# Kernel optimization log

Measured on AMD Instinct MI355X. Metric: run time of the kernel, lower is better.

## Reference

```python
import jax, jax.numpy as jnp
import numpy as np

B, SIG, L, LAT, ENC_H, DEC_H, RHS_H, T = 256, 64, 1024, 256, 256, 512, 512, 200


def setup_inputs() -> dict:
    key = jax.random.key(0)
    ks = jax.random.split(key, 32)
    p = lambda k, s: jax.random.normal(k, s, dtype=jnp.float32) * 0.05
    inp = {
        'y': jax.random.normal(ks[0], (B, SIG, L), dtype=jnp.float32),
        't': jnp.arange(T, dtype=jnp.float32) * 0.01,
        # encoder: conv3 (OIH) + bias, res conv1 + bias, 3 layers
        'ew0': p(ks[1], (ENC_H, SIG, 3)), 'eb0': p(ks[2], (ENC_H,)),
        'rw0': p(ks[3], (ENC_H, SIG, 1)), 'rb0': p(ks[4], (ENC_H,)),
        'ew1': p(ks[5], (ENC_H, ENC_H, 3)), 'eb1': p(ks[6], (ENC_H,)),
        'rw1': p(ks[7], (ENC_H, ENC_H, 1)), 'rb1': p(ks[8], (ENC_H,)),
        'ew2': p(ks[9], (LAT, ENC_H, 3)), 'eb2': p(ks[10], (LAT,)),
        'rw2': p(ks[11], (LAT, ENC_H, 1)), 'rb2': p(ks[12], (LAT,)),
        # rhs MLP: LAT -> RHS_H -> RHS_H -> LAT
        'fw0': p(ks[13], (RHS_H, LAT)), 'fb0': p(ks[14], (RHS_H,)),
        'fw1': p(ks[15], (RHS_H, RHS_H)), 'fb1': p(ks[16], (RHS_H,)),
        'fw2': p(ks[17], (LAT, RHS_H)), 'fb2': p(ks[18], (LAT,)),
        # decoder MLP: LAT -> DEC_H -> DEC_H -> SIG
        'dw0': p(ks[19], (DEC_H, LAT)), 'db0': p(ks[20], (DEC_H,)),
        'dw1': p(ks[21], (DEC_H, DEC_H)), 'db1': p(ks[22], (DEC_H,)),
        'dw2': p(ks[23], (SIG, DEC_H)), 'db2': p(ks[24], (SIG,)),
    }
    return inp


def _conv1d(x, w, b, pad):
    out = jax.lax.conv_general_dilated(x, w, window_strides=(1,), padding=[(pad, pad)],
                                       dimension_numbers=('NCH', 'OIH', 'NCH'))
    return out + b[None, :, None]


def _forward(y, t, ew0, eb0, rw0, rb0, ew1, eb1, rw1, rb1, ew2, eb2, rw2, rb2,
             fw0, fb0, fw1, fb1, fw2, fb2, dw0, db0, dw1, db1, dw2, db2):
    # --- encoder: residual conv blocks; tanh on all but last ---
    x = y
    for (cw, cb, rw, rb, act) in [(ew0, eb0, rw0, rb0, True),
                                  (ew1, eb1, rw1, rb1, True),
                                  (ew2, eb2, rw2, rb2, False)]:
        out = _conv1d(x, cw, cb, 1)
        x = _conv1d(x, rw, rb, 0) + out
        if act:
            x = jnp.tanh(x)
    z0 = x[:, :, 0]  # [B, LAT]

    # --- RHS MLP (autonomous) ---
    def rhs(z):
        h = jnp.tanh(z @ fw0.T + fb0)
        h = jnp.tanh(h @ fw1.T + fb1)
        return h @ fw2.T + fb2

    # --- fixed-grid RK4 odeint over t ---
    def step(z, ts):
        t0, t1 = ts
        h = t1 - t0
        k1 = rhs(z)
        k2 = rhs(z + 0.5 * h * k1)
        k3 = rhs(z + 0.5 * h * k2)
        k4 = rhs(z + h * k3)
        z = z + (h / 6.0) * (k1 + 2.0 * k2 + 2.0 * k3 + k4)
        return z, z

    _, zs = jax.lax.scan(step, z0, (t[:-1], t[1:]))
    pred_z = jnp.concatenate([z0[None], zs], axis=0)  # [T, B, LAT]

    # --- decoder MLP ---
    h = jnp.tanh(pred_z @ dw0.T + db0)
    h = jnp.tanh(h @ dw1.T + db1)
    pred_y = h @ dw2.T + db2  # [T, B, SIG]
    return jnp.transpose(pred_y, (1, 2, 0))  # [B, SIG, T]


def reference(y, t, ew0, eb0, rw0, rb0, ew1, eb1, rw1, rb1, ew2, eb2, rw2, rb2,
              fw0, fb0, fw1, fb1, fw2, fb2, dw0, db0, dw1, db1, dw2, db2):
    return _forward(y, t, ew0, eb0, rw0, rb0, ew1, eb1, rw1, rb1, ew2, eb2, rw2, rb2,
                    fw0, fb0, fw1, fb1, fw2, fb2, dw0, db0, dw1, db1, dw2, db2)
```

## Files before the change

### kernel.cpp

```cpp
#include <hip/hip_runtime.h>
#include <hip/hip_bf16.h>

typedef unsigned short u16;

#define B_      256
#define SIG_    64
#define L_      1024
#define LAT_    256
#define RHSH_   512
#define T_      200

__device__ __forceinline__ bool probe_bf16(const void* tptr) {
    return ((const unsigned*)tptr)[0] != 0u;
}
__device__ __forceinline__ float ld_flex(const void* p, size_t i, bool bf) {
    return bf ? __bfloat162float(((const __hip_bfloat16*)p)[i]) : ((const float*)p)[i];
}
__device__ __forceinline__ u16 f2bf(float f) {
    unsigned x = __float_as_uint(f);
    unsigned r = x + 0x7FFFu + ((x >> 16) & 1u);
    return (u16)(r >> 16);
}
__device__ __forceinline__ float bf2f(u16 v) {
    return __uint_as_float((unsigned)v << 16);
}

static constexpr size_t Z0F  = 0;
static constexpr size_t EW0T = Z0F  + 65536;
static constexpr size_t RW0T = EW0T + 49152;
static constexpr size_t EW1T = RW0T + 16384;
static constexpr size_t RW1T = EW1T + 196608;
static constexpr size_t EW2T = RW1T + 65536;
static constexpr size_t RW2T = EW2T + 196608;
static constexpr size_t CB0  = RW2T + 65536;
static constexpr size_t CB1  = CB0 + 256;
static constexpr size_t CB2  = CB1 + 256;
static constexpr size_t TFO  = CB2 + 256;
static constexpr size_t FB0  = TFO + 256;
static constexpr size_t FB1  = FB0 + 512;
static constexpr size_t FB2  = FB1 + 512;
static constexpr size_t DB0  = FB2 + 256;
static constexpr size_t DB1  = DB0 + 512;
static constexpr size_t DB2  = DB1 + 512;
static constexpr size_t SALT = DB2 + 64;
static constexpr size_t FP32_END = SALT + 16;

static constexpr size_t FW0NS = 0;
static constexpr size_t FW1NS = FW0NS + 131072;
static constexpr size_t FW2NS = FW1NS + 262144;
static constexpr size_t DW0B  = FW2NS + 131072;
static constexpr size_t DW1B  = DW0B + 131072;
static constexpr size_t DW2B  = DW1B + 262144;
static constexpr size_t ZS    = DW2B + 32768;
static constexpr size_t US_END = ZS + 13107200;

static constexpr size_t EXCH_U64_PER_PAIR = 2048;
static constexpr size_t EXCH_OFF  = FP32_END * 4 + US_END * 2;
static constexpr size_t EXCH_BYTES = 128 * EXCH_U64_PER_PAIR * 8;
static constexpr size_t NEED_BYTES = EXCH_OFF + EXCH_BYTES;

__global__ void k_transpose(const void* __restrict__ in, float* __restrict__ out,
                            int N, int K, const void* __restrict__ tp) {
    bool bf = probe_bf16(tp);
    int idx = blockIdx.x * 256 + threadIdx.x;
    if (idx < N * K) {
        int k = idx / N;
        int n = idx - k * N;
        out[idx] = ld_flex(in, (size_t)n * K + k, bf);
    }
}

__global__ void k_prep_wns(const void* __restrict__ in, u16* __restrict__ out,
                           int N, int K, const void* __restrict__ tp) {
    bool bf = probe_bf16(tp);
    int idx = blockIdx.x * 256 + threadIdx.x;
    if (idx >= N * K) return;
    int NH = N >> 1;
    int c = idx % NH;
    int k = (idx / NH) % K;
    int h = idx / (NH * K);
    float v = ld_flex(in, (size_t)(h * NH + c) * K + k, bf);
    out[idx] = f2bf(v);
}

__global__ void k_prep_wtb(const void* __restrict__ in, u16* __restrict__ out,
                           int N, int K, const void* __restrict__ tp) {
    bool bf = probe_bf16(tp);
    int idx = blockIdx.x * 256 + threadIdx.x;
    if (idx >= N * K) return;
    int n = idx % N;
    int k = idx / N;
    out[idx] = f2bf(ld_flex(in, (size_t)n * K + k, bf));
}

__global__ void k_cvt(const void* __restrict__ in, float* __restrict__ out, int n,
                      const void* __restrict__ tp) {
    bool bf = probe_bf16(tp);
    int i = blockIdx.x * 256 + threadIdx.x;
    if (i < n) out[i] = ld_flex(in, i, bf);
}

__global__ void k_cvt_add(const void* __restrict__ a, const void* __restrict__ b,
                          float* __restrict__ out, int n, const void* __restrict__ tp) {
    bool bf = probe_bf16(tp);
    int i = blockIdx.x * 256 + threadIdx.x;
    if (i < n) out[i] = ld_flex(a, i, bf) + ld_flex(b, i, bf);
}

__global__ void k_fill(float* __restrict__ out, int n, float v) {
    int i = blockIdx.x * 256 + threadIdx.x;
    if (i < n) out[i] = v;
}

__global__ void k_bump(unsigned* p) {
    if (threadIdx.x == 0) p[0] = p[0] + 1u;
}

__global__ __launch_bounds__(256) void k_encoder(
    const void* __restrict__ y, const void* __restrict__ tp,
    const float* __restrict__ ew0T, const float* __restrict__ rw0T, const float* __restrict__ cb0,
    const float* __restrict__ ew1T, const float* __restrict__ rw1T, const float* __restrict__ cb1,
    const float* __restrict__ ew2T, const float* __restrict__ rw2T, const float* __restrict__ cb2,
    float* __restrict__ z0f) {
    bool bf = probe_bf16(tp);
    int b = blockIdx.x;
    int o = threadIdx.x;
    __shared__ float ys[64][4];
    __shared__ float x1[3][256];
    __shared__ float x2[2][256];

    {
        int i = o >> 2, l = o & 3;
        ys[i][l] = ld_flex(y, (size_t)b * SIG_ * L_ + (size_t)i * L_ + l, bf);
    }
    __syncthreads();

    {
        float a0 = 0.f, a1 = 0.f, a2 = 0.f;
        for (int i = 0; i < 64; i++) {
            float w0 = ew0T[(i * 3 + 0) * 256 + o];
            float w1 = ew0T[(i * 3 + 1) * 256 + o];
            float w2 = ew0T[(i * 3 + 2) * 256 + o];
            float rw = rw0T[i * 256 + o];
            float v0 = ys[i][0], v1 = ys[i][1], v2 = ys[i][2], v3 = ys[i][3];
            a0 += w1 * v0 + w2 * v1 + rw * v0;
            a1 += w0 * v0 + w1 * v1 + w2 * v2 + rw * v1;
            a2 += w0 * v1 + w1 * v2 + w2 * v3 + rw * v2;
        }
        float cb = cb0[o];
        x1[0][o] = tanhf(a0 + cb);
        x1[1][o] = tanhf(a1 + cb);
        x1[2][o] = tanhf(a2 + cb);
    }
    __syncthreads();

    {
        float a0 = 0.f, a1 = 0.f;
        for (int i = 0; i < 256; i++) {
            float w0 = ew1T[(i * 3 + 0) * 256 + o];
            float w1 = ew1T[(i * 3 + 1) * 256 + o];
            float w2 = ew1T[(i * 3 + 2) * 256 + o];
            float rw = rw1T[i * 256 + o];
            float v0 = x1[0][i], v1 = x1[1][i], v2 = x1[2][i];
            a0 += w1 * v0 + w2 * v1 + rw * v0;
            a1 += w0 * v0 + w1 * v1 + w2 * v2 + rw * v1;
        }
        float cb = cb1[o];
        x2[0][o] = tanhf(a0 + cb);
        x2[1][o] = tanhf(a1 + cb);
    }
    __syncthreads();

    {
        float a0 = 0.f;
        for (int i = 0; i < 256; i++) {
            float w1 = ew2T[(i * 3 + 1) * 256 + o];
            float w2 = ew2T[(i * 3 + 2) * 256 + o];
            float rw = rw2T[i * 256 + o];
            a0 += w1 * x2[0][i] + w2 * x2[1][i] + rw * x2[0][i];
        }
        z0f[(size_t)b * 256 + o] = a0 + cb2[o];
    }
}

#define RM_NONE 0
#define RM_PLAIN 1
#define RM_S1 2
#define RM_S2 3
#define RM_S34 4
#define TL_PLAIN 0
#define TL_RK 1
#define TL_K4 2

template <int KIN, int NOUT, bool ACT, int RM, int TL>
__device__ __forceinline__ void layer_ns(
    float* xs,
    const u16* __restrict__ wb,
    const float* __restrict__ bias,
    float* xo,
    float* scratch,
    unsigned long long* __restrict__ sendBuf,
    const unsigned long long* __restrict__ recvBuf,
    unsigned sendTag, unsigned recvTag, int nHalf, int tid,
    float* zbL, float* acL, float* ztL,
    float rcAC, float rcZT,
    bool tInit, float tcAC, float tcZT,
    u16* zsOut) {
    constexpr int NH  = NOUT / 2;
    constexpr int CQ  = NH / 4;
    constexpr int NPH = 512 / CQ;
    constexpr int KH  = KIN / 2;
    constexpr int KC2 = KH / NPH;
    constexpr int WK  = KH / 8;
    const int cq = tid & (CQ - 1);
    const int ph = tid / CQ;
    const int locB = nHalf * KH;
    const int remB = KH - locB;
    const u16* wl = wb + ((size_t)(locB + ph * KC2)) * NH + 4 * cq;
    const u16* wr = wb + ((size_t)(remB + ph * KC2)) * NH + 4 * cq;
    const float* xl0 = xs + locB + ph * KC2;
    const float* xl1 = xs + KIN + locB + ph * KC2;
    float4 a0 = {0.f, 0.f, 0.f, 0.f}, a1 = {0.f, 0.f, 0.f, 0.f};
#pragma unroll 4
    for (int k = 0; k < KC2; k++) {
        uint2 w = *(const uint2*)(wl + (size_t)k * NH);
        float w0 = __uint_as_float(w.x << 16);
        float w1 = __uint_as_float(w.x & 0xFFFF0000u);
        float w2 = __uint_as_float(w.y << 16);
        float w3 = __uint_as_float(w.y & 0xFFFF0000u);
        float v0 = xl0[k], v1 = xl1[k];
        a0.x += v0 * w0; a0.y += v0 * w1; a0.z += v0 * w2; a0.w += v0 * w3;
        a1.x += v1 * w0; a1.y += v1 * w1; a1.z += v1 * w2; a1.w += v1 * w3;
    }
    if constexpr (RM != RM_NONE) {
        const int lane = tid & 63;
        const int wave = tid >> 6;
        if (lane < 2 * WK) {
            const int r = lane / WK;
            const int kRel = wave * WK + (lane % WK);
            unsigned long long p;
            for (;;) {
                p = __hip_atomic_load(&recvBuf[r * KH + kRel],
                                      __ATOMIC_RELAXED, __HIP_MEMORY_SCOPE_AGENT);
                if ((unsigned)(p >> 32) == recvTag) break;
                __builtin_amdgcn_s_sleep(2);
            }
            float kv = __uint_as_float((unsigned)p);
            const int xi = r * KIN + remB + kRel;
            if constexpr (RM == RM_PLAIN) {
                xs[xi] = kv;
            } else if constexpr (RM == RM_S1) {
                xs[xi] = acL[xi] + rcAC * kv;
            } else if constexpr (RM == RM_S2) {
                float zv = zbL[xi];
                acL[xi] = zv + rcAC * kv;
                xs[xi] = zv + rcZT * kv;
            } else {
                float zv = zbL[xi];
                acL[xi] += rcAC * kv;
                xs[xi] = zv + rcZT * kv;
            }
        }
    }
    const float* xr0 = xs + remB + ph * KC2;
    const float* xr1 = xs + KIN + remB + ph * KC2;
#pragma unroll 4
    for (int k = 0; k < KC2; k++) {
        uint2 w = *(const uint2*)(wr + (size_t)k * NH);
        float w0 = __uint_as_float(w.x << 16);
        float w1 = __uint_as_float(w.x & 0xFFFF0000u);
        float w2 = __uint_as_float(w.y << 16);
        float w3 = __uint_as_float(w.y & 0xFFFF0000u);
        float v0 = xr0[k], v1 = xr1[k];
        a0.x += v0 * w0; a0.y += v0 * w1; a0.z += v0 * w2; a0.w += v0 * w3;
        a1.x += v1 * w0; a1.y += v1 * w1; a1.z += v1 * w2; a1.w += v1 * w3;
    }
    *(float4*)(scratch + (size_t)(ph * 2 + 0) * NH + 4 * cq) = a0;
    *(float4*)(scratch + (size_t)(ph * 2 + 1) * NH + 4 * cq) = a1;
    __syncthreads();
    if (tid < 2 * NH) {
        const int r = tid / NH, c = tid % NH;
        float s = 0.f;
#pragma unroll
        for (int p = 0; p < NPH; p++) s += scratch[(size_t)(p * 2 + r) * NH + c];
        s += bias[c];
        if constexpr (TL == TL_PLAIN) {
            if (ACT) s = tanhf(s);
            xo[r * NOUT + nHalf * NH + c] = s;
        }
        {
            unsigned long long packed =
                ((unsigned long long)sendTag << 32) | (unsigned long long)__float_as_uint(s);
            __hip_atomic_store(&sendBuf[r * NH + c], packed,
                               __ATOMIC_RELAXED, __HIP_MEMORY_SCOPE_AGENT);
        }
        if constexpr (TL == TL_RK) {
            const int zi = r * 256 + nHalf * NH + c;
            float zv = zbL[zi];
            acL[zi] = (tInit ? zv : acL[zi]) + tcAC * s;
            ztL[zi] = zv + tcZT * s;
        } else if constexpr (TL == TL_K4) {
            const int zi = r * 256 + nHalf * NH + c;
            float zn = acL[zi] + tcAC * s;
            zbL[zi] = zn;
            zsOut[zi] = f2bf(zn);
        }
    }
    __syncthreads();
}

__global__ __launch_bounds__(512) void k_ode_ns(
    const u16* __restrict__ fw0ns, const float* __restrict__ fb0,
    const u16* __restrict__ fw1ns, const float* __restrict__ fb1,
    const u16* __restrict__ fw2ns, const float* __restrict__ fb2,
    const float* __restrict__ tf, const float* __restrict__ z0f,
    const unsigned* __restrict__ saltp,
    u16* __restrict__ zs, unsigned long long* __restrict__ ex) {
    __shared__ __align__(16) float zb[512];
    __shared__ __align__(16) float zt[512];
    __shared__ __align__(16) float ac[512];
    __shared__ __align__(16) float h1[1024];
    __shared__ __align__(16) float h2[1024];
    __shared__ __align__(16) float scratch[4096];

    const int tid = threadIdx.x;
    const int pairId = blockIdx.x & 127;
    const int nHalf  = blockIdx.x >> 7;
    const int row0 = pairId * 2;
    unsigned long long* exBase = ex + (size_t)pairId * EXCH_U64_PER_PAIR;

    const unsigned salt = __hip_atomic_load(saltp, __ATOMIC_RELAXED, __HIP_MEMORY_SCOPE_AGENT);
    unsigned tag = salt << 13;

#define SB(t) (exBase + ((size_t)(nHalf * 2 + ((t) & 1)) * 512))
#define RB(t) ((const unsigned long long*)(exBase + ((size_t)((1 - nHalf) * 2 + ((t) & 1)) * 512)))

    const u16* fw0w = fw0ns + (size_t)nHalf * 256 * 256;
    const u16* fw1w = fw1ns + (size_t)nHalf * 512 * 256;
    const u16* fw2w = fw2ns + (size_t)nHalf * 512 * 128;
    const float* fb0o = fb0 + nHalf * 256;
    const float* fb1o = fb1 + nHalf * 256;
    const float* fb2o = fb2 + nHalf * 128;

    zb[tid] = z0f[(size_t)(row0 + (tid >> 8)) * 256 + (tid & 255)];
    __syncthreads();

    if (tid < 256) {
        int r = tid >> 7, c = tid & 127;
        zs[(size_t)(row0 + r) * 256 + nHalf * 128 + c] = f2bf(zb[r * 256 + nHalf * 128 + c]);
    }

    float h6prev = 0.f;
    unsigned tcPrev = 0;

    for (int t = 0; t < T_ - 1; t++) {
        float hstep = tf[t + 1] - tf[t];
        float hh = 0.5f * hstep;
        float h3 = hstep * (1.0f / 3.0f);
        float h6 = hstep * (1.0f / 6.0f);

        unsigned ta, tb, tc;
        ta = ++tag; tb = ++tag; tc = ++tag;
        if (t == 0)
            layer_ns<256, 512, true, RM_NONE, TL_PLAIN>(zb, fw0w, fb0o, h1, scratch,
                SB(ta), nullptr, ta, 0u, nHalf, tid, zb, ac, zt, 0.f, 0.f, false, 0.f, 0.f, nullptr);
        else
            layer_ns<256, 512, true, RM_S1, TL_PLAIN>(zb, fw0w, fb0o, h1, scratch,
                SB(ta), RB(tcPrev), ta, tcPrev, nHalf, tid, zb, ac, zt, h6prev, 0.f, false, 0.f, 0.f, nullptr);
        layer_ns<512, 512, true, RM_PLAIN, TL_PLAIN>(h1, fw1w, fb1o, h2, scratch,
            SB(tb), RB(ta), tb, ta, nHalf, tid, zb, ac, zt, 0.f, 0.f, false, 0.f, 0.f, nullptr);
        layer_ns<512, 256, false, RM_PLAIN, TL_RK>(h2, fw2w, fb2o, nullptr, scratch,
            SB(tc), RB(tb), tc, tb, nHalf, tid, zb, ac, zt, 0.f, 0.f, true, h6, hh, nullptr);
        tcPrev = tc;

        ta = ++tag; tb = ++tag; tc = ++tag;
        layer_ns<256, 512, true, RM_S2, TL_PLAIN>(zt, fw0w, fb0o, h1, scratch,
            SB(ta), RB(tcPrev), ta, tcPrev, nHalf, tid, zb, ac, zt, h6, hh, false, 0.f, 0.f, nullptr);
        layer_ns<512, 512, true, RM_PLAIN, TL_PLAIN>(h1, fw1w, fb1o, h2, scratch,
            SB(tb), RB(ta), tb, ta, nHalf, tid, zb, ac, zt, 0.f, 0.f, false, 0.f, 0.f, nullptr);
        layer_ns<512, 256, false, RM_PLAIN, TL_RK>(h2, fw2w, fb2o, nullptr, scratch,
            SB(tc), RB(tb), tc, tb, nHalf, tid, zb, ac, zt, 0.f, 0.f, false, h3, hh, nullptr);
        tcPrev = tc;

        ta = ++tag; tb = ++tag; tc = ++tag;
        layer_ns<256, 512, true, RM_S34, TL_PLAIN>(zt, fw0w, fb0o, h1, scratch,
            SB(ta), RB(tcPrev), ta, tcPrev, nHalf, tid, zb, ac, zt, h3, hh, false, 0.f, 0.f, nullptr);
        layer_ns<512, 512, true, RM_PLAIN, TL_PLAIN>(h1, fw1w, fb1o, h2, scratch,
            SB(tb), RB(ta), tb, ta, nHalf, tid, zb, ac, zt, 0.f, 0.f, false, 0.f, 0.f, nullptr);
        layer_ns<512, 256, false, RM_PLAIN, TL_RK>(h2, fw2w, fb2o, nullptr, scratch,
            SB(tc), RB(tb), tc, tb, nHalf, tid, zb, ac, zt, 0.f, 0.f, false, h3, hstep, nullptr);
        tcPrev = tc;

        ta = ++tag; tb = ++tag; tc = ++tag;
        layer_ns<256, 512, true, RM_S34, TL_PLAIN>(zt, fw0w, fb0o, h1, scratch,
            SB(ta), RB(tcPrev), ta, tcPrev, nHalf, tid, zb, ac, zt, h3, hstep, false, 0.f, 0.f, nullptr);
        layer_ns<512, 512, true, RM_PLAIN, TL_PLAIN>(h1, fw1w, fb1o, h2, scratch,
            SB(tb), RB(ta), tb, ta, nHalf, tid, zb, ac, zt, 0.f, 0.f, false, 0.f, 0.f, nullptr);
        layer_ns<512, 256, false, RM_PLAIN, TL_K4>(h2, fw2w, fb2o, nullptr, scratch,
            SB(tc), RB(tb), tc, tb, nHalf, tid, zb, ac, zt, 0.f, 0.f, false, h6, 0.f,
            zs + (size_t)(t + 1) * 65536 + (size_t)row0 * 256);
        tcPrev = tc;
        h6prev = h6;
    }
#undef SB
#undef RB
}

template <int K>
__device__ __forceinline__ void dec_layer512(
    const float* xin, const u16* __restrict__ wt, const float* __restrict__ bias,
    float* xout, int tid) {
    const int q = tid & 127;
    const int g = tid >> 7;
    const u16* wp = wt + 4 * q;
    const float* xr = xin + (size_t)g * 5 * K;
    float4 a[5];
#pragma unroll
    for (int r = 0; r < 5; r++) a[r] = {0.f, 0.f, 0.f, 0.f};
#pragma unroll 4
    for (int k = 0; k < K; k++) {
        uint2 w = *(const uint2*)(wp + (size_t)k * 512);
        float w0 = __uint_as_float(w.x << 16);
        float w1 = __uint_as_float(w.x & 0xFFFF0000u);
        float w2 = __uint_as_float(w.y << 16);
        float w3 = __uint_as_float(w.y & 0xFFFF0000u);
#pragma unroll
        for (int r = 0; r < 5; r++) {
            float v = xr[r * K + k];
            a[r].x += v * w0; a[r].y += v * w1; a[r].z += v * w2; a[r].w += v * w3;
        }
    }
    float b0 = bias[4 * q + 0], b1 = bias[4 * q + 1], b2 = bias[4 * q + 2], b3 = bias[4 * q + 3];
#pragma unroll
    for (int r = 0; r < 5; r++) {
        float4 o;
        o.x = tanhf(a[r].x + b0);
        o.y = tanhf(a[r].y + b1);
        o.z = tanhf(a[r].z + b2);
        o.w = tanhf(a[r].w + b3);
        *(float4*)(xout + (size_t)(g * 5 + r) * 512 + 4 * q) = o;
    }
}

__global__ __launch_bounds__(512) void k_decode(
    const u16* __restrict__ zs,
    const u16* __restrict__ dw0b, const float* __restrict__ db0,
    const u16* __restrict__ dw1b, const float* __restrict__ db1,
    const u16* __restrict__ dw2b, const float* __restrict__ db2,
    float* __restrict__ out) {
    __shared__ __align__(16) float xb[20 * 256];
    __shared__ __align__(16) float hh1[20 * 512];
    __shared__ __align__(16) float hh2[20 * 512];
    const int tid = threadIdx.x;
    const int b  = blockIdx.x & 255;
    const int t0 = (blockIdx.x >> 8) * 20;

    for (int i = tid; i < 20 * 256; i += 512) {
        int r = i >> 8, k = i & 255;
        xb[i] = bf2f(zs[(size_t)(t0 + r) * 65536 + (size_t)b * 256 + k]);
    }
    __syncthreads();

    dec_layer512<256>(xb, dw0b, db0, hh1, tid);
    __syncthreads();
    dec_layer512<512>(hh1, dw1b, db1, hh2, tid);
    __syncthreads();

    if (tid < 320) {
        const int q = tid & 15;
        const int r = tid >> 4;
        const u16* wp = dw2b + 4 * q;
        const float* xr = hh2 + (size_t)r * 512;
        float4 a = {0.f, 0.f, 0.f, 0.f};
#pragma unroll 4
        for (int k = 0; k < 512; k++) {
            uint2 w = *(const uint2*)(wp + (size_t)k * 64);
            float w0 = __uint_as_float(w.x << 16);
            float w1 = __uint_as_float(w.x & 0xFFFF0000u);
            float w2 = __uint_as_float(w.y << 16);
            float w3 = __uint_as_float(w.y & 0xFFFF0000u);
            float v = xr[k];
            a.x += v * w0; a.y += v * w1; a.z += v * w2; a.w += v * w3;
        }
        const int tt = t0 + r;
        out[((size_t)b * 64 + 4 * q + 0) * 200 + tt] = a.x + db2[4 * q + 0];
        out[((size_t)b * 64 + 4 * q + 1) * 200 + tt] = a.y + db2[4 * q + 1];
        out[((size_t)b * 64 + 4 * q + 2) * 200 + tt] = a.z + db2[4 * q + 2];
        out[((size_t)b * 64 + 4 * q + 3) * 200 + tt] = a.w + db2[4 * q + 3];
    }
}

#define GRID256(n) ((((n) + 255) / 256))

static const int DICT_SIZES[26] = {
    16777216, 200, 49152, 256, 16384, 256, 196608, 256, 65536, 256,
    196608, 256, 65536, 256, 131072, 512, 262144, 512, 131072, 256,
    131072, 512, 262144, 512, 32768, 64};
static const int ALPHA_SIZES[26] = {
    512, 512, 64, 131072, 262144, 32768, 256, 256, 256, 49152,
    196608, 196608, 512, 512, 256, 131072, 262144, 131072, 256, 256,
    256, 16384, 65536, 65536, 200, 16777216};
static const int ALPHA_MAP[26] = {
    25, 24, 9, 6, 21, 18, 10, 7, 22, 19, 11, 8, 23, 20, 15, 12, 16, 13, 17, 14,
    3, 0, 4, 1, 5, 2};

extern "C" void kernel_launch(void* const* d_in, const int* in_sizes, int n_in,
                              void* d_out, int out_size, void* d_ws, size_t ws_size,
                              hipStream_t stream) {
    float* out = (float*)d_out;

    bool dict_ok = (n_in == 26), alpha_ok = (n_in == 26);
    for (int i = 0; i < 26 && i < n_in; i++) {
        if (in_sizes[i] != DICT_SIZES[i]) dict_ok = false;
        if (in_sizes[i] != ALPHA_SIZES[i]) alpha_ok = false;
    }
    const void* in[26];
    if (dict_ok) {
        for (int s = 0; s < 26; s++) in[s] = d_in[s];
    } else if (alpha_ok) {
        for (int s = 0; s < 26; s++) in[s] = d_in[ALPHA_MAP[s]];
    } else {
        k_fill<<<GRID256(out_size), 256, 0, stream>>>(out, out_size, 1000.0f);
        return;
    }
    if (ws_size < NEED_BYTES) {
        k_fill<<<GRID256(out_size), 256, 0, stream>>>(out, out_size, 500.0f);
        return;
    }

    const void* y   = in[0];
    const void* t   = in[1];
    const void* ew0 = in[2];
    const void* eb0 = in[3];
    const void* rw0 = in[4];
    const void* rb0 = in[5];
    const void* ew1 = in[6];
    const void* eb1 = in[7];
    const void* rw1 = in[8];
    const void* rb1 = in[9];
    const void* ew2 = in[10];
    const void* eb2 = in[11];
    const void* rw2 = in[12];
    const void* rb2 = in[13];
    const void* fw0 = in[14];
    const void* fb0 = in[15];
    const void* fw1 = in[16];
    const void* fb1 = in[17];
    const void* fw2 = in[18];
    const void* fb2 = in[19];
    const void* dw0 = in[20];
    const void* db0 = in[21];
    const void* dw1 = in[22];
    const void* db1 = in[23];
    const void* dw2 = in[24];
    const void* db2 = in[25];

    float* ws = (float*)d_ws;
    u16* wns = (u16*)(ws + FP32_END);
    unsigned long long* ex = (unsigned long long*)((char*)d_ws + EXCH_OFF);

    k_bump<<<1, 1, 0, stream>>>((unsigned*)(ws + SALT));

    k_transpose<<<GRID256(256 * 192), 256, 0, stream>>>(ew0, ws + EW0T, 256, 192, t);
    k_transpose<<<GRID256(256 * 64),  256, 0, stream>>>(rw0, ws + RW0T, 256, 64, t);
    k_transpose<<<GRID256(256 * 768), 256, 0, stream>>>(ew1, ws + EW1T, 256, 768, t);
    k_transpose<<<GRID256(256 * 256), 256, 0, stream>>>(rw1, ws + RW1T, 256, 256, t);
    k_transpose<<<GRID256(256 * 768), 256, 0, stream>>>(ew2, ws + EW2T, 256, 768, t);
    k_transpose<<<GRID256(256 * 256), 256, 0, stream>>>(rw2, ws + RW2T, 256, 256, t);

    k_prep_wns<<<GRID256(512 * 256), 256, 0, stream>>>(fw0, wns + FW0NS, 512, 256, t);
    k_prep_wns<<<GRID256(512 * 512), 256, 0, stream>>>(fw1, wns + FW1NS, 512, 512, t);
    k_prep_wns<<<GRID256(256 * 512), 256, 0, stream>>>(fw2, wns + FW2NS, 256, 512, t);
    k_prep_wtb<<<GRID256(512 * 256), 256, 0, stream>>>(dw0, wns + DW0B, 512, 256, t);
    k_prep_wtb<<<GRID256(512 * 512), 256, 0, stream>>>(dw1, wns + DW1B, 512, 512, t);
    k_prep_wtb<<<GRID256(64 * 512),  256, 0, stream>>>(dw2, wns + DW2B, 64, 512, t);

    k_cvt<<<GRID256(512), 256, 0, stream>>>(fb0, ws + FB0, 512, t);
    k_cvt<<<GRID256(512), 256, 0, stream>>>(fb1, ws + FB1, 512, t);
    k_cvt<<<GRID256(256), 256, 0, stream>>>(fb2, ws + FB2, 256, t);
    k_cvt<<<GRID256(512), 256, 0, stream>>>(db0, ws + DB0, 512, t);
    k_cvt<<<GRID256(512), 256, 0, stream>>>(db1, ws + DB1, 512, t);
    k_cvt<<<GRID256(64),  256, 0, stream>>>(db2, ws + DB2, 64, t);
    k_cvt<<<GRID256(200), 256, 0, stream>>>(t,   ws + TFO, 200, t);
    k_cvt_add<<<GRID256(256), 256, 0, stream>>>(eb0, rb0, ws + CB0, 256, t);
    k_cvt_add<<<GRID256(256), 256, 0, stream>>>(eb1, rb1, ws + CB1, 256, t);
    k_cvt_add<<<GRID256(256), 256, 0, stream>>>(eb2, rb2, ws + CB2, 256, t);

    k_encoder<<<B_, 256, 0, stream>>>(y, t,
        ws + EW0T, ws + RW0T, ws + CB0,
        ws + EW1T, ws + RW1T, ws + CB1,
        ws + EW2T, ws + RW2T, ws + CB2,
        ws + Z0F);

    k_ode_ns<<<256, 512, 0, stream>>>(
        wns + FW0NS, ws + FB0, wns + FW1NS, ws + FB1, wns + FW2NS, ws + FB2,
        ws + TFO, ws + Z0F, (const unsigned*)(ws + SALT),
        wns + ZS, ex);

    k_decode<<<2560, 512, 0, stream>>>(
        wns + ZS, wns + DW0B, ws + DB0, wns + DW1B, ws + DB1, wns + DW2B, ws + DB2, out);
}
```

Baseline: 9.128 ms.

## Switch RK4 MLP matvecs to fp16 packed dot2 with prefetched remote weights

Converts the RHS MLP weights to fp16 stored in k-pair-interleaved layout and computes the layer matvecs with v_dot2 fp16 instructions. Hidden activations are kept packed as half2 in shared memory, and the remote-half weights are loaded into registers before the cross-block exchange wait so the loads overlap the spin. tanh is replaced with an exp-based approximation in the RHS and decoder. The intent is to halve ALU work and shared-memory traffic on the sequential ODE critical path, at the cost of fp16 precision in a 200-step integration and more register pressure.

```diff
diff --git a/kernel.cpp b/kernel.cpp
--- a/kernel.cpp
+++ b/kernel.cpp
@@ -23,6 +23,32 @@
 }
 __device__ __forceinline__ float bf2f(u16 v) {
     return __uint_as_float((unsigned)v << 16);
+}
+
+typedef _Float16 half2_t __attribute__((ext_vector_type(2)));
+
+#if defined(__has_builtin)
+#if __has_builtin(__builtin_amdgcn_fdot2)
+#define HAVE_FDOT2 1
+#endif
+#endif
+
+__device__ __forceinline__ float fdot2(unsigned w, unsigned x, float c) {
+#ifdef HAVE_FDOT2
+    return __builtin_amdgcn_fdot2(__builtin_bit_cast(half2_t, w),
+                                  __builtin_bit_cast(half2_t, x), c, false);
+#else
+    half2_t a = __builtin_bit_cast(half2_t, w);
+    half2_t b = __builtin_bit_cast(half2_t, x);
+    return c + (float)a.x * (float)b.x + (float)a.y * (float)b.y;
+#endif
+}
+__device__ __forceinline__ unsigned pk16(float a, float b) {
+    return __builtin_bit_cast(unsigned, __builtin_amdgcn_cvt_pkrtz(a, b));
+}
+__device__ __forceinline__ float fast_tanh(float x) {
+    float e = __expf(2.0f * x);
+    return 1.0f - 2.0f / (e + 1.0f);
 }
 
 static constexpr size_t Z0F  = 0;
@@ -70,17 +96,21 @@
     }
 }
 
-__global__ void k_prep_wns(const void* __restrict__ in, u16* __restrict__ out,
-                           int N, int K, const void* __restrict__ tp) {
+__global__ void k_prep_wns16(const void* __restrict__ in, u16* __restrict__ out,
+                             int N, int K, const void* __restrict__ tp) {
     bool bf = probe_bf16(tp);
     int idx = blockIdx.x * 256 + threadIdx.x;
     if (idx >= N * K) return;
     int NH = N >> 1;
-    int c = idx % NH;
-    int k = (idx / NH) % K;
-    int h = idx / (NH * K);
+    int kp = idx & 1;
+    int c  = (idx >> 1) % NH;
+    int r  = (idx >> 1) / NH;
+    int k2 = r % (K >> 1);
+    int h  = r / (K >> 1);
+    int k  = 2 * k2 + kp;
     float v = ld_flex(in, (size_t)(h * NH + c) * K + k, bf);
-    out[idx] = f2bf(v);
+    _Float16 hv = (_Float16)v;
+    out[idx] = *(u16*)&hv;
 }
 
 __global__ void k_prep_wtb(const void* __restrict__ in, u16* __restrict__ out,
@@ -194,10 +224,11 @@
 
 template <int KIN, int NOUT, bool ACT, int RM, int TL>
 __device__ __forceinline__ void layer_ns(
-    float* xs,
-    const u16* __restrict__ wb,
+    float* zin,
+    unsigned* xpin,
+    const u16* __restrict__ wbu16,
     const float* __restrict__ bias,
-    float* xo,
+    unsigned* xpo,
     float* scratch,
     unsigned long long* __restrict__ sendBuf,
     const unsigned long long* __restrict__ recvBuf,
@@ -211,31 +242,60 @@
     constexpr int NPH = 512 / CQ;
     constexpr int KH  = KIN / 2;
     constexpr int KC2 = KH / NPH;
+    constexpr int K2C = KC2 / 2;
     constexpr int WK  = KH / 8;
+    constexpr bool ZIN = (RM != RM_PLAIN);
     const int cq = tid & (CQ - 1);
     const int ph = tid / CQ;
-    const int locB = nHalf * KH;
-    const int remB = KH - locB;
-    const u16* wl = wb + ((size_t)(locB + ph * KC2)) * NH + 4 * cq;
-    const u16* wr = wb + ((size_t)(remB + ph * KC2)) * NH + 4 * cq;
-    const float* xl0 = xs + locB + ph * KC2;
-    const float* xl1 = xs + KIN + locB + ph * KC2;
+    const int locB  = nHalf * KH;
+    const int remB  = KH - locB;
+    const int locB2 = locB >> 1;
+    const int remB2 = remB >> 1;
+    const unsigned* wb32 = (const unsigned*)wbu16;
+
+    uint4 wr4[K2C];
+    {
+        const unsigned* wr = wb32 + ((size_t)(remB2 + ph * K2C)) * NH + 4 * cq;
+#pragma unroll
+        for (int j = 0; j < K2C; j++) wr4[j] = *(const uint4*)(wr + (size_t)j * NH);
+    }
+
     float4 a0 = {0.f, 0.f, 0.f, 0.f}, a1 = {0.f, 0.f, 0.f, 0.f};
-#pragma unroll 4
-    for (int k = 0; k < KC2; k++) {
-        uint2 w = *(const uint2*)(wl + (size_t)k * NH);
-        float w0 = __uint_as_float(w.x << 16);
-        float w1 = __uint_as_float(w.x & 0xFFFF0000u);
-        float w2 = __uint_as_float(w.y << 16);
-        float w3 = __uint_as_float(w.y & 0xFFFF0000u);
-        float v0 = xl0[k], v1 = xl1[k];
-        a0.x += v0 * w0; a0.y += v0 * w1; a0.z += v0 * w2; a0.w += v0 * w3;
-        a1.x += v1 * w0; a1.y += v1 * w1; a1.z += v1 * w2; a1.w += v1 * w3;
-    }
+    {
+        const unsigned* wl = wb32 + ((size_t)(locB2 + ph * K2C)) * NH + 4 * cq;
+        if constexpr (ZIN) {
+            const float* zl0 = zin + locB + ph * KC2;
+            const float* zl1 = zin + KIN + locB + ph * KC2;
+#pragma unroll
+            for (int j = 0; j < K2C; j++) {
+                uint4 w4 = *(const uint4*)(wl + (size_t)j * NH);
+                float2 p0 = *(const float2*)(zl0 + 2 * j);
+                float2 p1 = *(const float2*)(zl1 + 2 * j);
+                unsigned x0 = pk16(p0.x, p0.y), x1 = pk16(p1.x, p1.y);
+                a0.x = fdot2(w4.x, x0, a0.x); a0.y = fdot2(w4.y, x0, a0.y);
+                a0.z = fdot2(w4.z, x0, a0.z); a0.w = fdot2(w4.w, x0, a0.w);
+                a1.x = fdot2(w4.x, x1, a1.x); a1.y = fdot2(w4.y, x1, a1.y);
+                a1.z = fdot2(w4.z, x1, a1.z); a1.w = fdot2(w4.w, x1, a1.w);
+            }
+        } else {
+            const unsigned* xq0 = xpin + locB2 + ph * K2C;
+            const unsigned* xq1 = xpin + KIN / 2 + locB2 + ph * K2C;
+#pragma unroll
+            for (int j = 0; j < K2C; j++) {
+                uint4 w4 = *(const uint4*)(wl + (size_t)j * NH);
+                unsigned x0 = xq0[j], x1 = xq1[j];
+                a0.x = fdot2(w4.x, x0, a0.x); a0.y = fdot2(w4.y, x0, a0.y);
+                a0.z = fdot2(w4.z, x0, a0.z); a0.w = fdot2(w4.w, x0, a0.w);
+                a1.x = fdot2(w4.x, x1, a1.x); a1.y = fdot2(w4.y, x1, a1.y);
+                a1.z = fdot2(w4.z, x1, a1.z); a1.w = fdot2(w4.w, x1, a1.w);
+            }
+        }
+    }
+
     if constexpr (RM != RM_NONE) {
         const int lane = tid & 63;
         const int wave = tid >> 6;
-        if (lane < 2 * WK) {
+        if constexpr (RM == RM_PLAIN) {
             const int r = lane / WK;
             const int kRel = wave * WK + (lane % WK);
             unsigned long long p;
@@ -246,35 +306,63 @@
                 __builtin_amdgcn_s_sleep(2);
             }
             float kv = __uint_as_float((unsigned)p);
-            const int xi = r * KIN + remB + kRel;
-            if constexpr (RM == RM_PLAIN) {
-                xs[xi] = kv;
-            } else if constexpr (RM == RM_S1) {
-                xs[xi] = acL[xi] + rcAC * kv;
-            } else if constexpr (RM == RM_S2) {
-                float zv = zbL[xi];
-                acL[xi] = zv + rcAC * kv;
-                xs[xi] = zv + rcZT * kv;
-            } else {
-                float zv = zbL[xi];
-                acL[xi] += rcAC * kv;
-                xs[xi] = zv + rcZT * kv;
+            float kn = __shfl_down(kv, 1);
+            if ((lane & 1) == 0)
+                xpin[r * (KIN / 2) + ((remB + kRel) >> 1)] = pk16(kv, kn);
+        } else {
+            if (lane < 2 * WK) {
+                const int r = lane / WK;
+                const int kRel = wave * WK + (lane % WK);
+                unsigned long long p;
+                for (;;) {
+                    p = __hip_atomic_load(&recvBuf[r * KH + kRel],
+                                          __ATOMIC_RELAXED, __HIP_MEMORY_SCOPE_AGENT);
+                    if ((unsigned)(p >> 32) == recvTag) break;
+                    __builtin_amdgcn_s_sleep(2);
+                }
+                float kv = __uint_as_float((unsigned)p);
+                const int xi = r * KIN + remB + kRel;
+                if constexpr (RM == RM_S1) {
+                    zin[xi] = acL[xi] + rcAC * kv;
+                } else if constexpr (RM == RM_S2) {
+                    float zv = zbL[xi];
+                    acL[xi] = zv + rcAC * kv;
+                    zin[xi] = zv + rcZT * kv;
+                } else {
+                    float zv = zbL[xi];
+                    acL[xi] += rcAC * kv;
+                    zin[xi] = zv + rcZT * kv;
+                }
             }
         }
     }
-    const float* xr0 = xs + remB + ph * KC2;
-    const float* xr1 = xs + KIN + remB + ph * KC2;
-#pragma unroll 4
-    for (int k = 0; k < KC2; k++) {
-        uint2 w = *(const uint2*)(wr + (size_t)k * NH);
-        float w0 = __uint_as_float(w.x << 16);
-        float w1 = __uint_as_float(w.x & 0xFFFF0000u);
-        float w2 = __uint_as_float(w.y << 16);
-        float w3 = __uint_as_float(w.y & 0xFFFF0000u);
-        float v0 = xr0[k], v1 = xr1[k];
-        a0.x += v0 * w0; a0.y += v0 * w1; a0.z += v0 * w2; a0.w += v0 * w3;
-        a1.x += v1 * w0; a1.y += v1 * w1; a1.z += v1 * w2; a1.w += v1 * w3;
-    }
+
+    if constexpr (ZIN) {
+        const float* zr0 = zin + remB + ph * KC2;
+        const float* zr1 = zin + KIN + remB + ph * KC2;
+#pragma unroll
+        for (int j = 0; j < K2C; j++) {
+            float2 p0 = *(const float2*)(zr0 + 2 * j);
+            float2 p1 = *(const float2*)(zr1 + 2 * j);
+            unsigned x0 = pk16(p0.x, p0.y), x1 = pk16(p1.x, p1.y);
+            a0.x = fdot2(wr4[j].x, x0, a0.x); a0.y = fdot2(wr4[j].y, x0, a0.y);
+            a0.z = fdot2(wr4[j].z, x0, a0.z); a0.w = fdot2(wr4[j].w, x0, a0.w);
+            a1.x = fdot2(wr4[j].x, x1, a1.x); a1.y = fdot2(wr4[j].y, x1, a1.y);
+            a1.z = fdot2(wr4[j].z, x1, a1.z); a1.w = fdot2(wr4[j].w, x1, a1.w);
+        }
+    } else {
+        const unsigned* xq0 = xpin + remB2 + ph * K2C;
+        const unsigned* xq1 = xpin + KIN / 2 + remB2 + ph * K2C;
+#pragma unroll
+        for (int j = 0; j < K2C; j++) {
+            unsigned x0 = xq0[j], x1 = xq1[j];
+            a0.x = fdot2(wr4[j].x, x0, a0.x); a0.y = fdot2(wr4[j].y, x0, a0.y);
+            a0.z = fdot2(wr4[j].z, x0, a0.z); a0.w = fdot2(wr4[j].w, x0, a0.w);
+            a1.x = fdot2(wr4[j].x, x1, a1.x); a1.y = fdot2(wr4[j].y, x1, a1.y);
+            a1.z = fdot2(wr4[j].z, x1, a1.z); a1.w = fdot2(wr4[j].w, x1, a1.w);
+        }
+    }
+
     *(float4*)(scratch + (size_t)(ph * 2 + 0) * NH + 4 * cq) = a0;
     *(float4*)(scratch + (size_t)(ph * 2 + 1) * NH + 4 * cq) = a1;
     __syncthreads();
@@ -284,22 +372,23 @@
 #pragma unroll
         for (int p = 0; p < NPH; p++) s += scratch[(size_t)(p * 2 + r) * NH + c];
         s += bias[c];
-        if constexpr (TL == TL_PLAIN) {
-            if (ACT) s = tanhf(s);
-            xo[r * NOUT + nHalf * NH + c] = s;
-        }
+        if (ACT) s = fast_tanh(s);
         {
             unsigned long long packed =
                 ((unsigned long long)sendTag << 32) | (unsigned long long)__float_as_uint(s);
             __hip_atomic_store(&sendBuf[r * NH + c], packed,
                                __ATOMIC_RELAXED, __HIP_MEMORY_SCOPE_AGENT);
         }
-        if constexpr (TL == TL_RK) {
+        if constexpr (TL == TL_PLAIN) {
+            float sn = __shfl_down(s, 1);
+            if ((tid & 1) == 0)
+                xpo[r * (NOUT / 2) + ((nHalf * NH + c) >> 1)] = pk16(s, sn);
+        } else if constexpr (TL == TL_RK) {
             const int zi = r * 256 + nHalf * NH + c;
             float zv = zbL[zi];
             acL[zi] = (tInit ? zv : acL[zi]) + tcAC * s;
             ztL[zi] = zv + tcZT * s;
-        } else if constexpr (TL == TL_K4) {
+        } else {
             const int zi = r * 256 + nHalf * NH + c;
             float zn = acL[zi] + tcAC * s;
             zbL[zi] = zn;
@@ -319,8 +408,8 @@
     __shared__ __align__(16) float zb[512];
     __shared__ __align__(16) float zt[512];
     __shared__ __align__(16) float ac[512];
-    __shared__ __align__(16) float h1[1024];
-    __shared__ __align__(16) float h2[1024];
+    __shared__ __align__(16) unsigned h1p[512];
+    __shared__ __align__(16) unsigned h2p[512];
     __shared__ __align__(16) float scratch[4096];
 
     const int tid = threadIdx.x;
@@ -335,9 +424,9 @@
 #define SB(t) (exBase + ((size_t)(nHalf * 2 + ((t) & 1)) * 512))
 #define RB(t) ((const unsigned long long*)(exBase + ((size_t)((1 - nHalf) * 2 + ((t) & 1)) * 512)))
 
-    const u16* fw0w = fw0ns + (size_t)nHalf * 256 * 256;
-    const u16* fw1w = fw1ns + (size_t)nHalf * 512 * 256;
-    const u16* fw2w = fw2ns + (size_t)nHalf * 512 * 128;
+    const u16* fw0w = fw0ns + (size_t)nHalf * 65536;
+    const u16* fw1w = fw1ns + (size_t)nHalf * 131072;
+    const u16* fw2w = fw2ns + (size_t)nHalf * 65536;
     const float* fb0o = fb0 + nHalf * 256;
     const float* fb1o = fb1 + nHalf * 256;
     const float* fb2o = fb2 + nHalf * 128;
@@ -362,41 +451,41 @@
         unsigned ta, tb, tc;
         ta = ++tag; tb = ++tag; tc = ++tag;
         if (t == 0)
-            layer_ns<256, 512, true, RM_NONE, TL_PLAIN>(zb, fw0w, fb0o, h1, scratch,
+            layer_ns<256, 512, true, RM_NONE, TL_PLAIN>(zb, nullptr, fw0w, fb0o, h1p, scratch,
                 SB(ta), nullptr, ta, 0u, nHalf, tid, zb, ac, zt, 0.f, 0.f, false, 0.f, 0.f, nullptr);
         else
-            layer_ns<256, 512, true, RM_S1, TL_PLAIN>(zb, fw0w, fb0o, h1, scratch,
+            layer_ns<256, 512, true, RM_S1, TL_PLAIN>(zb, nullptr, fw0w, fb0o, h1p, scratch,
                 SB(ta), RB(tcPrev), ta, tcPrev, nHalf, tid, zb, ac, zt, h6prev, 0.f, false, 0.f, 0.f, nullptr);
-        layer_ns<512, 512, true, RM_PLAIN, TL_PLAIN>(h1, fw1w, fb1o, h2, scratch,
+        layer_ns<512, 512, true, RM_PLAIN, TL_PLAIN>(nullptr, h1p, fw1w, fb1o, h2p, scratch,
             SB(tb), RB(ta), tb, ta, nHalf, tid, zb, ac, zt, 0.f, 0.f, false, 0.f, 0.f, nullptr);
-        layer_ns<512, 256, false, RM_PLAIN, TL_RK>(h2, fw2w, fb2o, nullptr, scratch,
+        layer_ns<512, 256, false, RM_PLAIN, TL_RK>(nullptr, h2p, fw2w, fb2o, nullptr, scratch,
             SB(tc), RB(tb), tc, tb, nHalf, tid, zb, ac, zt, 0.f, 0.f, true, h6, hh, nullptr);
         tcPrev = tc;
 
         ta = ++tag; tb = ++tag; tc = ++tag;
-        layer_ns<256, 512, true, RM_S2, TL_PLAIN>(zt, fw0w, fb0o, h1, scratch,
+        layer_ns<256, 512, true, RM_S2, TL_PLAIN>(zt, nullptr, fw0w, fb0o, h1p, scratch,
             SB(ta), RB(tcPrev), ta, tcPrev, nHalf, tid, zb, ac, zt, h6, hh, false, 0.f, 0.f, nullptr);
-        layer_ns<512, 512, true, RM_PLAIN, TL_PLAIN>(h1, fw1w, fb1o, h2, scratch,
+        layer_ns<512, 512, true, RM_PLAIN, TL_PLAIN>(nullptr, h1p, fw1w, fb1o, h2p, scratch,
             SB(tb), RB(ta), tb, ta, nHalf, tid, zb, ac, zt, 0.f, 0.f, false, 0.f, 0.f, nullptr);
-        layer_ns<512, 256, false, RM_PLAIN, TL_RK>(h2, fw2w, fb2o, nullptr, scratch,
+        layer_ns<512, 256, false, RM_PLAIN, TL_RK>(nullptr, h2p, fw2w, fb2o, nullptr, scratch,
             SB(tc), RB(tb), tc, tb, nHalf, tid, zb, ac, zt, 0.f, 0.f, false, h3, hh, nullptr);
         tcPrev = tc;
 
         ta = ++tag; tb = ++tag; tc = ++tag;
-        layer_ns<256, 512, true, RM_S34, TL_PLAIN>(zt, fw0w, fb0o, h1, scratch,
+        layer_ns<256, 512, true, RM_S34, TL_PLAIN>(zt, nullptr, fw0w, fb0o, h1p, scratch,
             SB(ta), RB(tcPrev), ta, tcPrev, nHalf, tid, zb, ac, zt, h3, hh, false, 0.f, 0.f, nullptr);
-        layer_ns<512, 512, true, RM_PLAIN, TL_PLAIN>(h1, fw1w, fb1o, h2, scratch,
+        layer_ns<512, 512, true, RM_PLAIN, TL_PLAIN>(nullptr, h1p, fw1w, fb1o, h2p, scratch,
             SB(tb), RB(ta), tb, ta, nHalf, tid, zb, ac, zt, 0.f, 0.f, false, 0.f, 0.f, nullptr);
-        layer_ns<512, 256, false, RM_PLAIN, TL_RK>(h2, fw2w, fb2o, nullptr, scratch,
+        layer_ns<512, 256, false, RM_PLAIN, TL_RK>(nullptr, h2p, fw2w, fb2o, nullptr, scratch,
             SB(tc), RB(tb), tc, tb, nHalf, tid, zb, ac, zt, 0.f, 0.f, false, h3, hstep, nullptr);
         tcPrev = tc;
 
         ta = ++tag; tb = ++tag; tc = ++tag;
-        layer_ns<256, 512, true, RM_S34, TL_PLAIN>(zt, fw0w, fb0o, h1, scratch,
+        layer_ns<256, 512, true, RM_S34, TL_PLAIN>(zt, nullptr, fw0w, fb0o, h1p, scratch,
             SB(ta), RB(tcPrev), ta, tcPrev, nHalf, tid, zb, ac, zt, h3, hstep, false, 0.f, 0.f, nullptr);
-        layer_ns<512, 512, true, RM_PLAIN, TL_PLAIN>(h1, fw1w, fb1o, h2, scratch,
+        layer_ns<512, 512, true, RM_PLAIN, TL_PLAIN>(nullptr, h1p, fw1w, fb1o, h2p, scratch,
             SB(tb), RB(ta), tb, ta, nHalf, tid, zb, ac, zt, 0.f, 0.f, false, 0.f, 0.f, nullptr);
-        layer_ns<512, 256, false, RM_PLAIN, TL_K4>(h2, fw2w, fb2o, nullptr, scratch,
+        layer_ns<512, 256, false, RM_PLAIN, TL_K4>(nullptr, h2p, fw2w, fb2o, nullptr, scratch,
             SB(tc), RB(tb), tc, tb, nHalf, tid, zb, ac, zt, 0.f, 0.f, false, h6, 0.f,
             zs + (size_t)(t + 1) * 65536 + (size_t)row0 * 256);
         tcPrev = tc;
@@ -434,10 +523,10 @@
 #pragma unroll
     for (int r = 0; r < 5; r++) {
         float4 o;
-        o.x = tanhf(a[r].x + b0);
-        o.y = tanhf(a[r].y + b1);
-        o.z = tanhf(a[r].z + b2);
-        o.w = tanhf(a[r].w + b3);
+        o.x = fast_tanh(a[r].x + b0);
+        o.y = fast_tanh(a[r].y + b1);
+        o.z = fast_tanh(a[r].z + b2);
+        o.w = fast_tanh(a[r].w + b3);
         *(float4*)(xout + (size_t)(g * 5 + r) * 512 + 4 * q) = o;
     }
 }
@@ -568,9 +657,9 @@
     k_transpose<<<GRID256(256 * 768), 256, 0, stream>>>(ew2, ws + EW2T, 256, 768, t);
     k_transpose<<<GRID256(256 * 256), 256, 0, stream>>>(rw2, ws + RW2T, 256, 256, t);
 
-    k_prep_wns<<<GRID256(512 * 256), 256, 0, stream>>>(fw0, wns + FW0NS, 512, 256, t);
-    k_prep_wns<<<GRID256(512 * 512), 256, 0, stream>>>(fw1, wns + FW1NS, 512, 512, t);
-    k_prep_wns<<<GRID256(256 * 512), 256, 0, stream>>>(fw2, wns + FW2NS, 256, 512, t);
+    k_prep_wns16<<<GRID256(512 * 256), 256, 0, stream>>>(fw0, wns + FW0NS, 512, 256, t);
+    k_prep_wns16<<<GRID256(512 * 512), 256, 0, stream>>>(fw1, wns + FW1NS, 512, 512, t);
+    k_prep_wns16<<<GRID256(256 * 512), 256, 0, stream>>>(fw2, wns + FW2NS, 256, 512, t);
     k_prep_wtb<<<GRID256(512 * 256), 256, 0, stream>>>(dw0, wns + DW0B, 512, 256, t);
     k_prep_wtb<<<GRID256(512 * 512), 256, 0, stream>>>(dw1, wns + DW1B, 512, 512, t);
     k_prep_wtb<<<GRID256(64 * 512),  256, 0, stream>>>(dw2, wns + DW2B, 64, 512, t);
```

After: 12.99 ms. +42.3%, slower.
